# Performance work log

Hardware: AMD Instinct MI355X
Metric: run time of the kernel (lower is better)

## Reference

```python
import jax, jax.numpy as jnp
import numpy as np


def _to_complex(x):
    # trailing axis holds (real, imag)
    return x[..., 0] + 1j * x[..., 1]


def _nufft2c(img, omega, csm):
    """Exact type-2 non-uniform DFT with coil sensitivities (reference for nufft2c_torch).

    img:   (H, W) real or complex image
    omega: (2, M) k-space coords in cycles/pixel, in [-0.5, 0.5]
    csm:   (C, H, W) complex coil sensitivity maps
    returns (C, M) complex k-space, centered & orthonormal-style 1/sqrt(HW) scaling.
    """
    H, W = img.shape
    y = jnp.arange(H, dtype=jnp.float32) - H / 2.0  # centered pixel coords
    z = jnp.arange(W, dtype=jnp.float32) - W / 2.0
    ey = jnp.exp(-2j * jnp.pi * omega[0][:, None] * y[None, :])  # (M, H)
    ez = jnp.exp(-2j * jnp.pi * omega[1][:, None] * z[None, :])  # (M, W)
    sim = csm * img[None, :, :].astype(csm.dtype)                # (C, H, W)
    tmp = jnp.einsum('chw,mw->cmh', sim, ez)                     # (C, M, H)
    k = jnp.einsum('cmh,mh->cm', tmp, ey) / np.float32(np.sqrt(H * W))
    return k


def setup_inputs() -> dict:
    key = jax.random.key(0)
    k0, k1, k2, k3, k4 = jax.random.split(key, 5)
    H = W = 300
    C = 4       # coils
    M = 4096    # non-Cartesian k-space samples
    img_pred = jax.random.normal(k0, (H, W, 1), jnp.float32)
    kdata = jax.random.normal(k1, (1, C, M, 2), jnp.float32)
    all_omega = jax.random.uniform(k2, (1, 2, M), jnp.float32) - 0.5  # cycles/pixel
    all_dcomp = jax.random.uniform(k3, (1, M), jnp.float32)
    all_csm = jax.random.normal(k4, (C, H, W, 2), jnp.float32)
    return {
        'img_pred': img_pred,
        'kdata': kdata,
        'all_omega': all_omega,
        'all_dcomp': all_dcomp,
        'all_csm': all_csm,
    }


def reference(img_pred, kdata, all_omega, all_dcomp, all_csm):
    Ncontrast = 1
    csm = _to_complex(all_csm)   # (C, H, W)
    kd = _to_complex(kdata)      # (Ncontrast, C, M)
    two_pi = jnp.float32(2.0 * np.pi)
    # radial k-space weighting, (Ncontrast, M)
    weight = jnp.sqrt((all_omega[:, 0, :] * two_pi) ** 2 +
                      (all_omega[:, 1, :] * two_pi) ** 2) + 1.0
    loss = jnp.float32(0.0)
    for ii in range(Ncontrast):
        img = img_pred[:, :, ii]                       # (H, W)
        ksp = _nufft2c(img, all_omega[ii], csm)        # (C, M)
        d = weight[ii][None, :] * (ksp - kd[ii])       # weighted complex residual
        # MSELoss over view_as_real == mean over all real & imag components
        loss = loss + jnp.mean(jnp.stack([d.real, d.imag]) ** 2)
    return loss
```

## Files before the change

kernel.cpp:

```cpp
#include <hip/hip_runtime.h>
#include <math.h>

#define HH 300
#define WW 300
#define CC 4
#define MM 4096
#define KP 640
#define NKC (KP/32)
#define CSTRIDE 384
#define MP (CC*CSTRIDE)
#define NP 8192
#define NRB (MP/128)

typedef __attribute__((ext_vector_type(4))) float f32x4;
typedef __attribute__((ext_vector_type(4))) int int4v;
typedef __attribute__((ext_vector_type(8))) int int8v;

#define TWO_PI 6.283185307179586f

__device__ __forceinline__ size_t cmaddr(int R, int row, int k) {
    return ((size_t)(k >> 5) * R + row) * 32 + (k & 31);
}

__device__ __forceinline__ float aval(const float* img, const float* csm,
                                      int c, int h, int k) {
    if (k >= 2 * WW) return 0.0f;
    int w = (k < WW) ? k : k - WW;
    float im = img[h * WW + w];
    const float* cs = csm + (((size_t)c * HH + h) * WW + w) * 2;
    return ((k < WW) ? cs[0] : cs[1]) * im;
}

__global__ __launch_bounds__(256) void prep_kernel(
    const float* __restrict__ img, const float* __restrict__ csm,
    const float* __restrict__ omega, unsigned char* __restrict__ A,
    unsigned char* __restrict__ B, float* __restrict__ out)
{
    const int bid = blockIdx.x;
    if (bid == 0 && threadIdx.x == 0) out[0] = 0.0f;
    const int ABLK = (MP * KP / 2) / 256;
    if (bid < ABLK) {
        int idx = bid * 256 + threadIdx.x;
        int row = idx / (KP / 2);
        int k   = (idx - row * (KP / 2)) * 2;
        int c = row / CSTRIDE;
        int h = row - c * CSTRIDE;
        float v0 = 0.0f, v1 = 0.0f;
        if (h < HH) { v0 = aval(img, csm, c, h, k); v1 = aval(img, csm, c, h, k + 1); }
        int pk = __builtin_amdgcn_cvt_pk_fp8_f32(v0, v1, 0, false);
        *(ushort*)(A + cmaddr(MP, row, k)) = (ushort)pk;
    } else {
        int idx = (bid - ABLK) * 256 + threadIdx.x;
        int m  = idx / 160;
        int wp = idx - m * 160;
        if (wp < 150) {
            int w = wp * 2;
            float om1 = omega[MM + m];
            float s0, c0, s1, c1;
            __sincosf(TWO_PI * om1 * (float)(w - 150), &s0, &c0);
            __sincosf(TWO_PI * om1 * (float)(w - 149), &s1, &c1);
            ushort rr = (ushort)__builtin_amdgcn_cvt_pk_fp8_f32(c0, c1, 0, false);
            ushort ii = (ushort)__builtin_amdgcn_cvt_pk_fp8_f32(-s0, -s1, 0, false);
            ushort ni = (ushort)__builtin_amdgcn_cvt_pk_fp8_f32(s0, s1, 0, false);
            *(ushort*)(B + cmaddr(NP, m,      w))        = rr;
            *(ushort*)(B + cmaddr(NP, m,      WW + w))   = ni;
            *(ushort*)(B + cmaddr(NP, m + MM, w))        = ii;
            *(ushort*)(B + cmaddr(NP, m + MM, WW + w))   = rr;
        } else {
            int k = 600 + (wp - 150) * 4;
            *(unsigned int*)(B + cmaddr(NP, m,      k)) = 0u;
            *(unsigned int*)(B + cmaddr(NP, m + MM, k)) = 0u;
        }
    }
}

__global__ __launch_bounds__(256) void gemm_kernel(
    const unsigned char* __restrict__ A, const unsigned char* __restrict__ B,
    const float* __restrict__ omega, float2* __restrict__ P)
{
    __shared__ float2 red[128];

    const int t    = threadIdx.x;
    const int wave = t >> 6;
    const int ln   = t & 63;
    const int row0 = blockIdx.y * 128;
    const int col0 = blockIdx.x * 128;
    const int wr = wave >> 1, wc = wave & 1;
    const int lr = ln & 15;
    const int lq = ln >> 4;

    if (t < 128) red[t] = make_float2(0.0f, 0.0f);

    const int arow = row0 + wr * 64 + lr;
    const int bcol = col0 + wc * 64 + lr;

    f32x4 acc[4][4] = {};

    #pragma unroll
    for (int kc = 0; kc < NKC; kc += 4) {
        int8v a[4], b[4];
        #pragma unroll
        for (int i = 0; i < 4; ++i) {
            const unsigned char* pA = A + ((size_t)(kc + lq) * MP + arow + i * 16) * 32;
            int4v lo = *(const int4v*)pA;
            int4v hi = *(const int4v*)(pA + 16);
            a[i] = __builtin_shufflevector(lo, hi, 0, 1, 2, 3, 4, 5, 6, 7);
        }
        #pragma unroll
        for (int j = 0; j < 4; ++j) {
            const unsigned char* pB = B + ((size_t)(kc + lq) * NP + bcol + j * 16) * 32;
            int4v lo = *(const int4v*)pB;
            int4v hi = *(const int4v*)(pB + 16);
            b[j] = __builtin_shufflevector(lo, hi, 0, 1, 2, 3, 4, 5, 6, 7);
        }
        #pragma unroll
        for (int i = 0; i < 4; ++i)
            #pragma unroll
            for (int j = 0; j < 4; ++j)
                acc[i][j] = __builtin_amdgcn_mfma_scale_f32_16x16x128_f8f6f4(
                    a[i], b[j], acc[i][j], 0, 0,
                    0, 0x7f7f7f7f, 0, 0x7f7f7f7f);
    }

    __syncthreads();

    const int c  = row0 / CSTRIDE;
    const int h0 = row0 - c * CSTRIDE;

    #pragma unroll
    for (int j = 0; j < 4; ++j) {
        const int jcol = wc * 64 + j * 16 + lr;
        const int m = (col0 + jcol) & (MM - 1);
        const float om0 = omega[m];
        float ss, sc;
        __sincosf(TWO_PI * om0, &ss, &sc);
        const float str = sc, sti = -ss;
        float s2r = str * str - sti * sti, s2i = 2.0f * str * sti;
        float s4r = s2r * s2r - s2i * s2i, s4i = 2.0f * s2r * s2i;
        float s8r = s4r * s4r - s4i * s4i, s8i = 2.0f * s4r * s4i;
        float s16r = s8r * s8r - s8i * s8i, s16i = 2.0f * s8r * s8i;

        const int hb0 = h0 + wr * 64 + lq * 4;
        float sn, cs;
        __sincosf(TWO_PI * om0 * (float)(hb0 - 150), &sn, &cs);
        float byr = cs, byi = -sn;

        float pr = 0.0f, pi = 0.0f;
        #pragma unroll
        for (int i = 0; i < 4; ++i) {
            float er = byr, ei = byi;
            #pragma unroll
            for (int r = 0; r < 4; ++r) {
                const float v = acc[i][j][r];
                pr = fmaf(v, er, pr);
                pi = fmaf(v, ei, pi);
                float nr = er * str - ei * sti;
                ei = er * sti + ei * str;
                er = nr;
            }
            float nbr = byr * s16r - byi * s16i;
            byi = byr * s16i + byi * s16r;
            byr = nbr;
        }
        pr += __shfl_down(pr, 32); pi += __shfl_down(pi, 32);
        pr += __shfl_down(pr, 16); pi += __shfl_down(pi, 16);
        if (lq == 0) {
            atomicAdd(&red[jcol].x, pr);
            atomicAdd(&red[jcol].y, pi);
        }
    }
    __syncthreads();

    if (t < 128) {
        const int rb = row0 >> 7;
        P[(size_t)rb * NP + col0 + t] = red[t];
    }
}

__global__ __launch_bounds__(64) void loss_kernel(
    const float2* __restrict__ P, const float* __restrict__ kdata,
    const float* __restrict__ omega, float* __restrict__ out)
{
    const int t = blockIdx.x * 64 + threadIdx.x;
    const int c = t >> 12;
    const int m = t & (MM - 1);

    float kr = 0.0f, ki = 0.0f;
    #pragma unroll
    for (int q = 0; q < 3; ++q) {
        const int rb = 3 * c + q;
        float2 p0 = P[(size_t)rb * NP + m];
        float2 p1 = P[(size_t)rb * NP + m + MM];
        kr += p0.x - p1.y;
        ki += p0.y + p1.x;
    }
    kr *= (1.0f / 300.0f);
    ki *= (1.0f / 300.0f);

    const float om0 = omega[m];
    const float om1 = omega[MM + m];
    const size_t kidx = ((size_t)c * MM + m) * 2;
    const float kdr = kdata[kidx];
    const float kdi = kdata[kidx + 1];
    const float w0 = om0 * TWO_PI, w1 = om1 * TWO_PI;
    const float wg = sqrtf(w0 * w0 + w1 * w1) + 1.0f;
    const float dr = wg * (kr - kdr);
    const float di = wg * (ki - kdi);
    float val = (dr * dr + di * di) * (1.0f / (2.0f * CC * MM));

    #pragma unroll
    for (int off = 32; off > 0; off >>= 1) val += __shfl_down(val, off);
    if (threadIdx.x == 0) atomicAdd(out, val);
}

extern "C" void kernel_launch(void* const* d_in, const int* in_sizes, int n_in,
                              void* d_out, int out_size, void* d_ws, size_t ws_size,
                              hipStream_t stream) {
    const float* img   = (const float*)d_in[0];
    const float* kdata = (const float*)d_in[1];
    const float* omega = (const float*)d_in[2];
    const float* csm   = (const float*)d_in[4];
    float* out = (float*)d_out;

    unsigned char* Aws = (unsigned char*)d_ws;
    unsigned char* Bws = (unsigned char*)d_ws + (1u << 20);
    float2*        Pws = (float2*)((char*)d_ws + (8u << 20));

    const int ablk = (MP * KP / 2) / 256;
    const int bblk = (MM * 160) / 256;
    prep_kernel<<<ablk + bblk, 256, 0, stream>>>(img, csm, omega, Aws, Bws, out);
    gemm_kernel<<<dim3(NP / 128, MP / 128), 256, 0, stream>>>(Aws, Bws, omega, Pws);
    loss_kernel<<<CC * MM / 64, 64, 0, stream>>>(Pws, kdata, omega, out);
}
```

Before: 84.02 us.

## Pack coil rows densely, halve GEMM column tile, vectorize prep writes

Coil rows are now packed contiguously (1280 padded rows instead of 4x384), which removes wasted GEMM rows. Row blocks that straddle two coils split their epilogue into two partial outputs, and the loss kernel sums them through small index tables. The GEMM column tile drops from 128 to 64, which doubles the number of blocks. The prep kernel writes 4-byte words per thread with a coalesced layout, at the cost of more sincos calls per thread for B.

```diff
diff --git a/kernel.cpp b/kernel.cpp
--- a/kernel.cpp
+++ b/kernel.cpp
@@ -7,8 +7,7 @@
 #define MM 4096
 #define KP 640
 #define NKC (KP/32)
-#define CSTRIDE 384
-#define MP (CC*CSTRIDE)
+#define MP 1280
 #define NP 8192
 #define NRB (MP/128)
 
@@ -17,19 +16,6 @@
 typedef __attribute__((ext_vector_type(8))) int int8v;
 
 #define TWO_PI 6.283185307179586f
-
-__device__ __forceinline__ size_t cmaddr(int R, int row, int k) {
-    return ((size_t)(k >> 5) * R + row) * 32 + (k & 31);
-}
-
-__device__ __forceinline__ float aval(const float* img, const float* csm,
-                                      int c, int h, int k) {
-    if (k >= 2 * WW) return 0.0f;
-    int w = (k < WW) ? k : k - WW;
-    float im = img[h * WW + w];
-    const float* cs = csm + (((size_t)c * HH + h) * WW + w) * 2;
-    return ((k < WW) ? cs[0] : cs[1]) * im;
-}
 
 __global__ __launch_bounds__(256) void prep_kernel(
     const float* __restrict__ img, const float* __restrict__ csm,
@@ -37,68 +23,94 @@
     unsigned char* __restrict__ B, float* __restrict__ out)
 {
     const int bid = blockIdx.x;
-    if (bid == 0 && threadIdx.x == 0) out[0] = 0.0f;
-    const int ABLK = (MP * KP / 2) / 256;
-    if (bid < ABLK) {
-        int idx = bid * 256 + threadIdx.x;
-        int row = idx / (KP / 2);
-        int k   = (idx - row * (KP / 2)) * 2;
-        int c = row / CSTRIDE;
-        int h = row - c * CSTRIDE;
-        float v0 = 0.0f, v1 = 0.0f;
-        if (h < HH) { v0 = aval(img, csm, c, h, k); v1 = aval(img, csm, c, h, k + 1); }
-        int pk = __builtin_amdgcn_cvt_pk_fp8_f32(v0, v1, 0, false);
-        *(ushort*)(A + cmaddr(MP, row, k)) = (ushort)pk;
+    const int t   = threadIdx.x;
+    if (bid == 0 && t == 0) out[0] = 0.0f;
+    const int lane = t & 63;
+    const int jj   = lane & 7;
+    const int rl   = lane >> 3;
+
+    if (bid < 800) {
+        int gw = (bid * 256 + t) >> 6;
+        int kc = gw / 160;
+        int row = (gw - kc * 160) * 8 + rl;
+        int k0 = kc * 32 + jj * 4;
+        unsigned int word = 0;
+        if (row < CC * HH) {
+            int c = row / HH;
+            int h = row - c * HH;
+            float v[4];
+            #pragma unroll
+            for (int q = 0; q < 4; ++q) {
+                int k = k0 + q;
+                float vv = 0.0f;
+                if (k < 2 * WW) {
+                    int w = (k < WW) ? k : k - WW;
+                    float im = img[h * WW + w];
+                    const float* cs = csm + (((size_t)c * HH + h) * WW + w) * 2;
+                    vv = ((k < WW) ? cs[0] : cs[1]) * im;
+                }
+                v[q] = vv;
+            }
+            unsigned int lo = (unsigned int)(ushort)__builtin_amdgcn_cvt_pk_fp8_f32(v[0], v[1], 0, false);
+            unsigned int hi = (unsigned int)(ushort)__builtin_amdgcn_cvt_pk_fp8_f32(v[2], v[3], 0, false);
+            word = lo | (hi << 16);
+        }
+        *(unsigned int*)(A + ((size_t)kc * MP + row) * 32 + jj * 4) = word;
     } else {
-        int idx = (bid - ABLK) * 256 + threadIdx.x;
-        int m  = idx / 160;
-        int wp = idx - m * 160;
-        if (wp < 150) {
-            int w = wp * 2;
-            float om1 = omega[MM + m];
-            float s0, c0, s1, c1;
-            __sincosf(TWO_PI * om1 * (float)(w - 150), &s0, &c0);
-            __sincosf(TWO_PI * om1 * (float)(w - 149), &s1, &c1);
-            ushort rr = (ushort)__builtin_amdgcn_cvt_pk_fp8_f32(c0, c1, 0, false);
-            ushort ii = (ushort)__builtin_amdgcn_cvt_pk_fp8_f32(-s0, -s1, 0, false);
-            ushort ni = (ushort)__builtin_amdgcn_cvt_pk_fp8_f32(s0, s1, 0, false);
-            *(ushort*)(B + cmaddr(NP, m,      w))        = rr;
-            *(ushort*)(B + cmaddr(NP, m,      WW + w))   = ni;
-            *(ushort*)(B + cmaddr(NP, m + MM, w))        = ii;
-            *(ushort*)(B + cmaddr(NP, m + MM, WW + w))   = rr;
-        } else {
-            int k = 600 + (wp - 150) * 4;
-            *(unsigned int*)(B + cmaddr(NP, m,      k)) = 0u;
-            *(unsigned int*)(B + cmaddr(NP, m + MM, k)) = 0u;
-        }
+        int gw = ((bid - 800) * 256 + t) >> 6;
+        int kc = gw / 512;
+        int m  = (gw - kc * 512) * 8 + rl;
+        int k0 = kc * 32 + jj * 4;
+        float om1 = omega[MM + m];
+        float p0[4], p1[4];
+        #pragma unroll
+        for (int q = 0; q < 4; ++q) {
+            int k = k0 + q;
+            float a0 = 0.0f, a1 = 0.0f;
+            if (k < 2 * WW) {
+                int w = (k < WW) ? k : k - WW;
+                float s, c;
+                __sincosf(TWO_PI * om1 * (float)(w - 150), &s, &c);
+                a0 = (k < WW) ? c : s;
+                a1 = (k < WW) ? -s : c;
+            }
+            p0[q] = a0; p1[q] = a1;
+        }
+        unsigned int lo0 = (unsigned int)(ushort)__builtin_amdgcn_cvt_pk_fp8_f32(p0[0], p0[1], 0, false);
+        unsigned int hi0 = (unsigned int)(ushort)__builtin_amdgcn_cvt_pk_fp8_f32(p0[2], p0[3], 0, false);
+        unsigned int lo1 = (unsigned int)(ushort)__builtin_amdgcn_cvt_pk_fp8_f32(p1[0], p1[1], 0, false);
+        unsigned int hi1 = (unsigned int)(ushort)__builtin_amdgcn_cvt_pk_fp8_f32(p1[2], p1[3], 0, false);
+        *(unsigned int*)(B + ((size_t)kc * NP + m) * 32 + jj * 4)      = lo0 | (hi0 << 16);
+        *(unsigned int*)(B + ((size_t)kc * NP + m + MM) * 32 + jj * 4) = lo1 | (hi1 << 16);
     }
 }
 
 __global__ __launch_bounds__(256) void gemm_kernel(
     const unsigned char* __restrict__ A, const unsigned char* __restrict__ B,
-    const float* __restrict__ omega, float2* __restrict__ P)
+    const float* __restrict__ omega, float2* __restrict__ P2)
 {
-    __shared__ float2 red[128];
+    __shared__ float2 red[2][64];
 
     const int t    = threadIdx.x;
     const int wave = t >> 6;
     const int ln   = t & 63;
     const int row0 = blockIdx.y * 128;
-    const int col0 = blockIdx.x * 128;
-    const int wr = wave >> 1, wc = wave & 1;
+    const int col0 = blockIdx.x * 64;
+    const int wr = wave >> 1;
+    const int wc = wave & 1;
     const int lr = ln & 15;
     const int lq = ln >> 4;
 
-    if (t < 128) red[t] = make_float2(0.0f, 0.0f);
+    if (t < 64) { red[0][t] = make_float2(0.f, 0.f); red[1][t] = make_float2(0.f, 0.f); }
 
     const int arow = row0 + wr * 64 + lr;
-    const int bcol = col0 + wc * 64 + lr;
-
-    f32x4 acc[4][4] = {};
+    const int bcol = col0 + wc * 32 + lr;
+
+    f32x4 acc[4][2] = {};
 
     #pragma unroll
     for (int kc = 0; kc < NKC; kc += 4) {
-        int8v a[4], b[4];
+        int8v a[4], b[2];
         #pragma unroll
         for (int i = 0; i < 4; ++i) {
             const unsigned char* pA = A + ((size_t)(kc + lq) * MP + arow + i * 16) * 32;
@@ -107,7 +119,7 @@
             a[i] = __builtin_shufflevector(lo, hi, 0, 1, 2, 3, 4, 5, 6, 7);
         }
         #pragma unroll
-        for (int j = 0; j < 4; ++j) {
+        for (int j = 0; j < 2; ++j) {
             const unsigned char* pB = B + ((size_t)(kc + lq) * NP + bcol + j * 16) * 32;
             int4v lo = *(const int4v*)pB;
             int4v hi = *(const int4v*)(pB + 16);
@@ -116,7 +128,7 @@
         #pragma unroll
         for (int i = 0; i < 4; ++i)
             #pragma unroll
-            for (int j = 0; j < 4; ++j)
+            for (int j = 0; j < 2; ++j)
                 acc[i][j] = __builtin_amdgcn_mfma_scale_f32_16x16x128_f8f6f4(
                     a[i], b[j], acc[i][j], 0, 0,
                     0, 0x7f7f7f7f, 0, 0x7f7f7f7f);
@@ -124,78 +136,84 @@
 
     __syncthreads();
 
-    const int c  = row0 / CSTRIDE;
-    const int h0 = row0 - c * CSTRIDE;
+    const int cmin   = row0 / HH;
+    const int cbound = (cmin + 1) * HH;
 
     #pragma unroll
-    for (int j = 0; j < 4; ++j) {
-        const int jcol = wc * 64 + j * 16 + lr;
+    for (int j = 0; j < 2; ++j) {
+        const int jcol = wc * 32 + j * 16 + lr;
         const int m = (col0 + jcol) & (MM - 1);
         const float om0 = omega[m];
         float ss, sc;
         __sincosf(TWO_PI * om0, &ss, &sc);
         const float str = sc, sti = -ss;
-        float s2r = str * str - sti * sti, s2i = 2.0f * str * sti;
-        float s4r = s2r * s2r - s2i * s2i, s4i = 2.0f * s2r * s2i;
-        float s8r = s4r * s4r - s4i * s4i, s8i = 2.0f * s4r * s4i;
-        float s16r = s8r * s8r - s8i * s8i, s16i = 2.0f * s8r * s8i;
-
-        const int hb0 = h0 + wr * 64 + lq * 4;
-        float sn, cs;
-        __sincosf(TWO_PI * om0 * (float)(hb0 - 150), &sn, &cs);
-        float byr = cs, byi = -sn;
-
-        float pr = 0.0f, pi = 0.0f;
+
+        float p0r = 0.f, p0i = 0.f, p1r = 0.f, p1i = 0.f;
         #pragma unroll
         for (int i = 0; i < 4; ++i) {
-            float er = byr, ei = byi;
+            const int g  = row0 + wr * 64 + i * 16 + lq * 4;
+            const bool hi = (g >= cbound);
+            const int h  = g - (hi ? cbound : cmin * HH);
+            float sn, cs;
+            __sincosf(TWO_PI * om0 * (float)(h - 150), &sn, &cs);
+            float er = cs, ei = -sn;
+            float qr = 0.f, qi = 0.f;
             #pragma unroll
             for (int r = 0; r < 4; ++r) {
                 const float v = acc[i][j][r];
-                pr = fmaf(v, er, pr);
-                pi = fmaf(v, ei, pi);
+                qr = fmaf(v, er, qr);
+                qi = fmaf(v, ei, qi);
                 float nr = er * str - ei * sti;
                 ei = er * sti + ei * str;
                 er = nr;
             }
-            float nbr = byr * s16r - byi * s16i;
-            byi = byr * s16i + byi * s16r;
-            byr = nbr;
-        }
-        pr += __shfl_down(pr, 32); pi += __shfl_down(pi, 32);
-        pr += __shfl_down(pr, 16); pi += __shfl_down(pi, 16);
+            p0r += hi ? 0.f : qr;  p0i += hi ? 0.f : qi;
+            p1r += hi ? qr : 0.f;  p1i += hi ? qi : 0.f;
+        }
+        p0r += __shfl_down(p0r, 32); p0i += __shfl_down(p0i, 32);
+        p1r += __shfl_down(p1r, 32); p1i += __shfl_down(p1i, 32);
+        p0r += __shfl_down(p0r, 16); p0i += __shfl_down(p0i, 16);
+        p1r += __shfl_down(p1r, 16); p1i += __shfl_down(p1i, 16);
         if (lq == 0) {
-            atomicAdd(&red[jcol].x, pr);
-            atomicAdd(&red[jcol].y, pi);
+            atomicAdd(&red[0][jcol].x, p0r);
+            atomicAdd(&red[0][jcol].y, p0i);
+            atomicAdd(&red[1][jcol].x, p1r);
+            atomicAdd(&red[1][jcol].y, p1i);
         }
     }
     __syncthreads();
 
-    if (t < 128) {
-        const int rb = row0 >> 7;
-        P[(size_t)rb * NP + col0 + t] = red[t];
+    if (t < 64) {
+        const int rb = blockIdx.y;
+        P2[(size_t)(rb * 2 + 0) * NP + col0 + t] = red[0][t];
+        P2[(size_t)(rb * 2 + 1) * NP + col0 + t] = red[1][t];
     }
 }
 
 __global__ __launch_bounds__(64) void loss_kernel(
-    const float2* __restrict__ P, const float* __restrict__ kdata,
+    const float2* __restrict__ P2, const float* __restrict__ kdata,
     const float* __restrict__ omega, float* __restrict__ out)
 {
+    const int cnt[4] = {3, 3, 4, 3};
+    const int off[4] = {0, 3, 6, 10};
+    const int ent[13] = {0, 2, 4,  5, 6, 8,  9, 10, 12, 14,  15, 16, 18};
+
     const int t = blockIdx.x * 64 + threadIdx.x;
     const int c = t >> 12;
     const int m = t & (MM - 1);
 
-    float kr = 0.0f, ki = 0.0f;
-    #pragma unroll
-    for (int q = 0; q < 3; ++q) {
-        const int rb = 3 * c + q;
-        float2 p0 = P[(size_t)rb * NP + m];
-        float2 p1 = P[(size_t)rb * NP + m + MM];
-        kr += p0.x - p1.y;
-        ki += p0.y + p1.x;
-    }
-    kr *= (1.0f / 300.0f);
-    ki *= (1.0f / 300.0f);
+    float2 krc = make_float2(0.f, 0.f);
+    float2 kic = make_float2(0.f, 0.f);
+    const int e0 = off[c], n = cnt[c];
+    for (int e = e0; e < e0 + n; ++e) {
+        const size_t base = (size_t)ent[e] * NP;
+        float2 p0 = P2[base + m];
+        float2 p1 = P2[base + m + MM];
+        krc.x += p0.x; krc.y += p0.y;
+        kic.x += p1.x; kic.y += p1.y;
+    }
+    float kr = (krc.x - kic.y) * (1.0f / 300.0f);
+    float ki = (krc.y + kic.x) * (1.0f / 300.0f);
 
     const float om0 = omega[m];
     const float om1 = omega[MM + m];
@@ -209,7 +227,7 @@
     float val = (dr * dr + di * di) * (1.0f / (2.0f * CC * MM));
 
     #pragma unroll
-    for (int off = 32; off > 0; off >>= 1) val += __shfl_down(val, off);
+    for (int o = 32; o > 0; o >>= 1) val += __shfl_down(val, o);
     if (threadIdx.x == 0) atomicAdd(out, val);
 }
 
@@ -224,11 +242,9 @@
 
     unsigned char* Aws = (unsigned char*)d_ws;
     unsigned char* Bws = (unsigned char*)d_ws + (1u << 20);
-    float2*        Pws = (float2*)((char*)d_ws + (8u << 20));
-
-    const int ablk = (MP * KP / 2) / 256;
-    const int bblk = (MM * 160) / 256;
-    prep_kernel<<<ablk + bblk, 256, 0, stream>>>(img, csm, omega, Aws, Bws, out);
-    gemm_kernel<<<dim3(NP / 128, MP / 128), 256, 0, stream>>>(Aws, Bws, omega, Pws);
-    loss_kernel<<<CC * MM / 64, 64, 0, stream>>>(Pws, kdata, omega, out);
-}
+    float2*        P2  = (float2*)((char*)d_ws + (8u << 20));
+
+    prep_kernel<<<800 + 2560, 256, 0, stream>>>(img, csm, omega, Aws, Bws, out);
+    gemm_kernel<<<dim3(NP / 64, MP / 128), 256, 0, stream>>>(Aws, Bws, omega, P2);
+    loss_kernel<<<CC * MM / 64, 64, 0, stream>>>(P2, kdata, omega, out);
+}
```

Result: slower. 86.83 us (+3.3%).
